# Kernel tuning notes

Measured on AMD Instinct MI355X. Metric: run time of the kernel, lower is better.

## Reference

```python
import jax, jax.numpy as jnp
import numpy as np

N = 4096       # rows (batch * points)
D = 512        # d_model
H = 8          # num_heads


def setup_inputs() -> dict:
    key = jax.random.key(0)
    ks = jax.random.split(key, 11)
    s = 1.0 / np.sqrt(D).astype(np.float32)
    return {
        "x_q": jax.random.normal(ks[0], (N, D), jnp.float32),
        "x_k": jax.random.normal(ks[1], (N, D), jnp.float32),
        "x_v": jax.random.normal(ks[2], (N, D), jnp.float32),
        "Wq": jax.random.normal(ks[3], (D, D), jnp.float32) * s,
        "bq": jax.random.normal(ks[4], (D,), jnp.float32) * s,
        "Wk": jax.random.normal(ks[5], (D, D), jnp.float32) * s,
        "bk": jax.random.normal(ks[6], (D,), jnp.float32) * s,
        "Wv": jax.random.normal(ks[7], (D, D), jnp.float32) * s,
        "bv": jax.random.normal(ks[8], (D,), jnp.float32) * s,
        "Wo": jax.random.normal(ks[9], (D, D), jnp.float32) * s,
        "bo": jax.random.normal(ks[10], (D,), jnp.float32) * s,
    }


def reference(x_q, x_k, x_v, Wq, bq, Wk, bk, Wv, bv, Wo, bo):
    n, d = x_q.shape
    d_k = d // H
    # linear projections
    q = (x_q @ Wq + bq).reshape(n, H, d_k)  # chunk(dim=-1) == head split
    k = (x_k @ Wk + bk).reshape(n, H, d_k)
    v = (x_v @ Wv + bv).reshape(n, H, d_k)
    # channel-wise outer-product attention: scores[n,h,i,j] = q_i * k_j / sqrt(d_k)
    scale = jnp.asarray(1.0 / np.sqrt(d_k), q.dtype)
    scores = q[..., :, None] * k[..., None, :] * scale  # (n, H, d_k, d_k)
    p = jax.nn.softmax(scores, axis=-1)
    # attn output: p @ v over channel axis -> (n, H, d_k)
    x = jnp.einsum('nhij,nhj->nhi', p, v).reshape(n, d)  # head merge (cat dim=-1)
    return (x_q - x) @ Wo + bo
```

## Files before the change

### kernel.cpp

```cpp
#include <hip/hip_runtime.h>
#include <hip/hip_bf16.h>

#define NROWS 4096
#define DMODEL 512
#define NHEAD 8
#define DKH 64
#define ND (NROWS * DMODEL)
#define DD (DMODEL * DMODEL)

typedef unsigned short u16;
typedef __attribute__((ext_vector_type(8))) short short8;
typedef __attribute__((ext_vector_type(4))) float floatx4;

__device__ __forceinline__ u16 f2b(float f) {
    unsigned u = __float_as_uint(f);
    unsigned r = (u + 0x7fffu + ((u >> 16) & 1u)) >> 16;
    return (u16)r;
}
__device__ __forceinline__ float b2f(u16 v) {
    return __uint_as_float(((unsigned)v) << 16);
}
__device__ __forceinline__ void async16(const void* g, void* l) {
    __builtin_amdgcn_global_load_lds(g, l, 16, 0, 0);
}
__device__ __forceinline__ short8 cvt8(float4 a0, float4 a1) {
    short8 av;
    av[0] = f2b(a0.x); av[1] = f2b(a0.y); av[2] = f2b(a0.z); av[3] = f2b(a0.w);
    av[4] = f2b(a1.x); av[5] = f2b(a1.y); av[6] = f2b(a1.z); av[7] = f2b(a1.w);
    return av;
}

__global__ __launch_bounds__(256) void prep(
    const float* __restrict__ W0, const float* __restrict__ W1,
    const float* __restrict__ W2, const float* __restrict__ W3,
    u16* __restrict__ T0, u16* __restrict__ T1, u16* __restrict__ T2,
    u16* __restrict__ T3, const float* __restrict__ x0,
    const float* __restrict__ x1, const float* __restrict__ x2,
    u16* __restrict__ y0, u16* __restrict__ y1, u16* __restrict__ y2) {
    const int bid = blockIdx.x;
    const int tid = threadIdx.x;
    if (bid < 1024) {
        __shared__ float tile[32][33];
        int z = bid >> 8, t = bid & 255;
        const float* W = z == 0 ? W0 : (z == 1 ? W1 : (z == 2 ? W2 : W3));
        u16* T = z == 0 ? T0 : (z == 1 ? T1 : (z == 2 ? T2 : T3));
        int n0 = (t & 15) * 32, k0 = (t >> 4) * 32;
        int tx = tid & 31, ty = tid >> 5;
#pragma unroll
        for (int r = 0; r < 32; r += 8)
            tile[ty + r][tx] = W[(size_t)(k0 + ty + r) * DMODEL + n0 + tx];
        __syncthreads();
#pragma unroll
        for (int r = 0; r < 32; r += 8)
            T[(size_t)(n0 + ty + r) * DMODEL + k0 + tx] = f2b(tile[tx][ty + r]);
    } else {
        int b = bid - 1024;
        int zz = b >> 10;
        const float* s = zz == 0 ? x0 : (zz == 1 ? x1 : x2);
        u16* d = zz == 0 ? y0 : (zz == 1 ? y1 : y2);
        int i = (b & 1023) * 2048 + tid * 8;
        float4 a0 = *(const float4*)(s + i);
        float4 a1 = *(const float4*)(s + i + 4);
        *(short8*)(d + i) = cvt8(a0, a1);
    }
}

__global__ __launch_bounds__(256, 3) void proj3(
    const u16* __restrict__ xqb, const u16* __restrict__ xkb,
    const u16* __restrict__ xvb, const u16* __restrict__ wtq,
    const u16* __restrict__ wtk, const u16* __restrict__ wtv,
    const float* __restrict__ bq, const float* __restrict__ bk,
    const float* __restrict__ bv, u16* __restrict__ Q, u16* __restrict__ K,
    u16* __restrict__ V) {
    __shared__ __align__(16) u16 sA[2][64 * 32];
    __shared__ __align__(16) u16 sB[2][128 * 32];

    const int d = blockIdx.x;
    const int id = (d & 7) * 96 + (d >> 3);
    const int z = id >> 8;
    const int t2 = id & 255;
    const int tileM = (t2 >> 2) * 64;
    const int tileN = (t2 & 3) * 128;

    const u16* A = z == 0 ? xqb : (z == 1 ? xkb : xvb);
    const u16* Bt = z == 0 ? wtq : (z == 1 ? wtk : wtv);
    const float* bias = z == 0 ? bq : (z == 1 ? bk : bv);
    u16* C = z == 0 ? Q : (z == 1 ? K : V);

    const int tid = threadIdx.x;
    const int wave = tid >> 6, lane = tid & 63;
    const int wm = wave >> 1, wn = wave & 1;
    const int lr4 = lane >> 2, ls = lane & 3;
    const int lrow = lane & 15, sk = lane >> 4;

    const int ra = wave * 16 + lr4;
    const int sa = ls ^ ((ra >> 1) & 3);
    const u16* aptr = A + (size_t)(tileM + ra) * 512 + sa * 8;
    const int rb0 = (wave * 2) * 16 + lr4;
    const int rb1 = (wave * 2 + 1) * 16 + lr4;
    const int sb0 = ls ^ ((rb0 >> 1) & 3);
    const int sb1 = ls ^ ((rb1 >> 1) & 3);
    const u16* bptr0 = Bt + (size_t)(tileN + rb0) * 512 + sb0 * 8;
    const u16* bptr1 = Bt + (size_t)(tileN + rb1) * 512 + sb1 * 8;

    floatx4 acc[2][4];
#pragma unroll
    for (int i = 0; i < 2; i++)
#pragma unroll
        for (int j = 0; j < 4; j++) acc[i][j] = (floatx4){0.f, 0.f, 0.f, 0.f};

    async16(aptr, &sA[0][wave * 512]);
    async16(bptr0, &sB[0][wave * 1024]);
    async16(bptr1, &sB[0][wave * 1024 + 512]);
    __syncthreads();

    for (int t = 0; t < 16; ++t) {
        const int cur = t & 1, nxt = cur ^ 1;
        if (t < 15) {
            async16(aptr + (t + 1) * 32, &sA[nxt][wave * 512]);
            async16(bptr0 + (t + 1) * 32, &sB[nxt][wave * 1024]);
            async16(bptr1 + (t + 1) * 32, &sB[nxt][wave * 1024 + 512]);
        }
        short8 afr[2], bfr[4];
#pragma unroll
        for (int mi = 0; mi < 2; ++mi) {
            int r = wm * 32 + mi * 16 + lrow;
            int s = sk ^ ((r >> 1) & 3);
            afr[mi] = *(const short8*)&sA[cur][r * 32 + s * 8];
        }
#pragma unroll
        for (int ni = 0; ni < 4; ++ni) {
            int r = wn * 64 + ni * 16 + lrow;
            int s = sk ^ ((r >> 1) & 3);
            bfr[ni] = *(const short8*)&sB[cur][r * 32 + s * 8];
        }
#pragma unroll
        for (int mi = 0; mi < 2; ++mi)
#pragma unroll
            for (int ni = 0; ni < 4; ++ni)
                acc[mi][ni] = __builtin_amdgcn_mfma_f32_16x16x32_bf16(
                    afr[mi], bfr[ni], acc[mi][ni], 0, 0, 0);
        __syncthreads();
    }

#pragma unroll
    for (int mi = 0; mi < 2; ++mi)
#pragma unroll
        for (int ni = 0; ni < 4; ++ni) {
            int col = tileN + wn * 64 + ni * 16 + lrow;
            float bv_ = bias[col];
#pragma unroll
            for (int r2 = 0; r2 < 4; r2++) {
                int row = tileM + wm * 32 + mi * 16 + sk * 4 + r2;
                C[(size_t)row * 512 + col] = f2b(acc[mi][ni][r2] + bv_);
            }
        }
}

__global__ __launch_bounds__(256) void attn_kernel(
    const u16* __restrict__ Qb, const u16* __restrict__ Kb,
    const u16* __restrict__ Vb, const float* __restrict__ xq,
    u16* __restrict__ Tout) {
    __shared__ float lk[4][64];
    __shared__ float lv[4][64];
    const int wave = threadIdx.x >> 6, lane = threadIdx.x & 63;
    const int p = blockIdx.x * 4 + wave;
    const int n = p >> 3, h = p & 7;
    const size_t base = (size_t)n * DMODEL + h * DKH;

    float qi = b2f(Qb[base + lane]) * 0.125f;
    lk[wave][lane] = b2f(Kb[base + lane]);
    lv[wave][lane] = b2f(Vb[base + lane]);
    __syncthreads();

    float num = 0.f, den = 0.f;
#pragma unroll
    for (int j = 0; j < 64; j += 4) {
        float4 kv = *(const float4*)&lk[wave][j];
        float4 vv = *(const float4*)&lv[wave][j];
        float e0 = __expf(qi * kv.x);
        float e1 = __expf(qi * kv.y);
        float e2 = __expf(qi * kv.z);
        float e3 = __expf(qi * kv.w);
        den += e0 + e1 + e2 + e3;
        num += e0 * vv.x + e1 * vv.y + e2 * vv.z + e3 * vv.w;
    }
    float t = xq[base + lane] - num / den;
    Tout[base + lane] = f2b(t);
}

__global__ __launch_bounds__(256, 2) void out_gemm(const u16* __restrict__ T,
                                                   const u16* __restrict__ wto,
                                                   const float* __restrict__ bo,
                                                   float* __restrict__ C) {
    __shared__ __align__(16) u16 sA[2][2048];
    __shared__ __align__(16) u16 sB[2][2048];
    const int d = blockIdx.x;
    const int id = (d & 7) * 64 + (d >> 3);
    const int tileM = (id >> 3) * 64;
    const int tileN = (id & 7) * 64;

    const int tid = threadIdx.x;
    const int wave = tid >> 6, lane = tid & 63;
    const int wm = wave >> 1, wn = wave & 1;
    const int lr4 = lane >> 2, ls = lane & 3;
    const int lrow = lane & 15, sk = lane >> 4;

    const int r0 = wave * 16 + lr4;
    const int s0 = ls ^ ((r0 >> 1) & 3);
    const u16* aptr = T + (size_t)(tileM + r0) * 512 + s0 * 8;
    const u16* bptr = wto + (size_t)(tileN + r0) * 512 + s0 * 8;

    floatx4 acc[2][2];
#pragma unroll
    for (int i = 0; i < 2; i++)
#pragma unroll
        for (int j = 0; j < 2; j++) acc[i][j] = (floatx4){0.f, 0.f, 0.f, 0.f};

    async16(aptr, &sA[0][wave * 512]);
    async16(bptr, &sB[0][wave * 512]);
    __syncthreads();

    for (int t = 0; t < 16; ++t) {
        const int cur = t & 1, nxt = cur ^ 1;
        if (t < 15) {
            async16(aptr + (t + 1) * 32, &sA[nxt][wave * 512]);
            async16(bptr + (t + 1) * 32, &sB[nxt][wave * 512]);
        }
        short8 afr[2], bfr[2];
#pragma unroll
        for (int mi = 0; mi < 2; ++mi) {
            int r = wm * 32 + mi * 16 + lrow;
            int s = sk ^ ((r >> 1) & 3);
            afr[mi] = *(const short8*)&sA[cur][r * 32 + s * 8];
        }
#pragma unroll
        for (int ni = 0; ni < 2; ++ni) {
            int r = wn * 32 + ni * 16 + lrow;
            int s = sk ^ ((r >> 1) & 3);
            bfr[ni] = *(const short8*)&sB[cur][r * 32 + s * 8];
        }
#pragma unroll
        for (int mi = 0; mi < 2; ++mi)
#pragma unroll
            for (int ni = 0; ni < 2; ++ni)
                acc[mi][ni] = __builtin_amdgcn_mfma_f32_16x16x32_bf16(
                    afr[mi], bfr[ni], acc[mi][ni], 0, 0, 0);
        __syncthreads();
    }

#pragma unroll
    for (int mi = 0; mi < 2; ++mi)
#pragma unroll
        for (int ni = 0; ni < 2; ++ni) {
            int col = tileN + wn * 32 + ni * 16 + lrow;
            float bv = bo[col];
#pragma unroll
            for (int r2 = 0; r2 < 4; r2++) {
                int row = tileM + wm * 32 + mi * 16 + sk * 4 + r2;
                C[(size_t)row * 512 + col] = acc[mi][ni][r2] + bv;
            }
        }
}

extern "C" void kernel_launch(void* const* d_in, const int* in_sizes, int n_in,
                              void* d_out, int out_size, void* d_ws,
                              size_t ws_size, hipStream_t stream) {
    const float* x_q = (const float*)d_in[0];
    const float* x_k = (const float*)d_in[1];
    const float* x_v = (const float*)d_in[2];
    const float* Wq = (const float*)d_in[3];
    const float* bq = (const float*)d_in[4];
    const float* Wk = (const float*)d_in[5];
    const float* bk = (const float*)d_in[6];
    const float* Wv = (const float*)d_in[7];
    const float* bv = (const float*)d_in[8];
    const float* Wo = (const float*)d_in[9];
    const float* bo = (const float*)d_in[10];

    u16* ws = (u16*)d_ws;
    u16* xqb = ws;
    u16* xkb = xqb + ND;
    u16* xvb = xkb + ND;
    u16* wtq = xvb + ND;
    u16* wtk = wtq + DD;
    u16* wtv = wtk + DD;
    u16* wto = wtv + DD;
    u16* Qb = wto + DD;
    u16* Kb = Qb + ND;
    u16* Vb = Kb + ND;
    u16* Tb = Vb + ND;

    prep<<<dim3(4096), 256, 0, stream>>>(Wq, Wk, Wv, Wo, wtq, wtk, wtv, wto,
                                         x_q, x_k, x_v, xqb, xkb, xvb);
    proj3<<<dim3(768), 256, 0, stream>>>(xqb, xkb, xvb, wtq, wtk, wtv, bq, bk,
                                         bv, Qb, Kb, Vb);
    attn_kernel<<<dim3(NROWS * NHEAD / 4), 256, 0, stream>>>(Qb, Kb, Vb, x_q,
                                                             Tb);
    out_gemm<<<dim3(512), 256, 0, stream>>>(Tb, wto, bo, (float*)d_out);
}
```

Before: 138.5 us.

## Fuse fp32-to-bf16 input conversion into projection GEMM and double K tile

The projection GEMM now reads x_q/x_k/x_v as fp32 directly from global memory. It converts them to bf16 in registers and writes them into swizzled LDS, so the separate conversion pass and its bf16 workspace round trip are gone. Both GEMMs move from a K-step of 32 to 64, which halves the number of barriers and loop iterations but doubles LDS use per block. The A operand for the next tile is loaded into registers before the MFMAs and stored after them, which adds register pressure and the cost of reading fp32 directly.

New measurement: 135.3 us, median of 2. 1.02x faster.

```diff
diff --git a/kernel.cpp b/kernel.cpp
--- a/kernel.cpp
+++ b/kernel.cpp
@@ -30,50 +30,35 @@
     return av;
 }
 
-__global__ __launch_bounds__(256) void prep(
+__global__ __launch_bounds__(256) void prep_w(
     const float* __restrict__ W0, const float* __restrict__ W1,
     const float* __restrict__ W2, const float* __restrict__ W3,
     u16* __restrict__ T0, u16* __restrict__ T1, u16* __restrict__ T2,
-    u16* __restrict__ T3, const float* __restrict__ x0,
-    const float* __restrict__ x1, const float* __restrict__ x2,
-    u16* __restrict__ y0, u16* __restrict__ y1, u16* __restrict__ y2) {
-    const int bid = blockIdx.x;
-    const int tid = threadIdx.x;
-    if (bid < 1024) {
-        __shared__ float tile[32][33];
-        int z = bid >> 8, t = bid & 255;
-        const float* W = z == 0 ? W0 : (z == 1 ? W1 : (z == 2 ? W2 : W3));
-        u16* T = z == 0 ? T0 : (z == 1 ? T1 : (z == 2 ? T2 : T3));
-        int n0 = (t & 15) * 32, k0 = (t >> 4) * 32;
-        int tx = tid & 31, ty = tid >> 5;
-#pragma unroll
-        for (int r = 0; r < 32; r += 8)
-            tile[ty + r][tx] = W[(size_t)(k0 + ty + r) * DMODEL + n0 + tx];
-        __syncthreads();
-#pragma unroll
-        for (int r = 0; r < 32; r += 8)
-            T[(size_t)(n0 + ty + r) * DMODEL + k0 + tx] = f2b(tile[tx][ty + r]);
-    } else {
-        int b = bid - 1024;
-        int zz = b >> 10;
-        const float* s = zz == 0 ? x0 : (zz == 1 ? x1 : x2);
-        u16* d = zz == 0 ? y0 : (zz == 1 ? y1 : y2);
-        int i = (b & 1023) * 2048 + tid * 8;
-        float4 a0 = *(const float4*)(s + i);
-        float4 a1 = *(const float4*)(s + i + 4);
-        *(short8*)(d + i) = cvt8(a0, a1);
-    }
+    u16* __restrict__ T3) {
+    __shared__ float tile[32][33];
+    const int z = blockIdx.x >> 8, t = blockIdx.x & 255;
+    const float* W = z == 0 ? W0 : (z == 1 ? W1 : (z == 2 ? W2 : W3));
+    u16* T = z == 0 ? T0 : (z == 1 ? T1 : (z == 2 ? T2 : T3));
+    int n0 = (t & 15) * 32, k0 = (t >> 4) * 32;
+    int tx = threadIdx.x & 31, ty = threadIdx.x >> 5;
+#pragma unroll
+    for (int r = 0; r < 32; r += 8)
+        tile[ty + r][tx] = W[(size_t)(k0 + ty + r) * DMODEL + n0 + tx];
+    __syncthreads();
+#pragma unroll
+    for (int r = 0; r < 32; r += 8)
+        T[(size_t)(n0 + ty + r) * DMODEL + k0 + tx] = f2b(tile[tx][ty + r]);
 }
 
 __global__ __launch_bounds__(256, 3) void proj3(
-    const u16* __restrict__ xqb, const u16* __restrict__ xkb,
-    const u16* __restrict__ xvb, const u16* __restrict__ wtq,
+    const float* __restrict__ xq, const float* __restrict__ xk,
+    const float* __restrict__ xv, const u16* __restrict__ wtq,
     const u16* __restrict__ wtk, const u16* __restrict__ wtv,
     const float* __restrict__ bq, const float* __restrict__ bk,
     const float* __restrict__ bv, u16* __restrict__ Q, u16* __restrict__ K,
     u16* __restrict__ V) {
-    __shared__ __align__(16) u16 sA[2][64 * 32];
-    __shared__ __align__(16) u16 sB[2][128 * 32];
+    __shared__ __align__(16) u16 sA[2][64 * 64];
+    __shared__ __align__(16) u16 sB[2][128 * 64];
 
     const int d = blockIdx.x;
     const int id = (d & 7) * 96 + (d >> 3);
@@ -82,7 +67,7 @@
     const int tileM = (t2 >> 2) * 64;
     const int tileN = (t2 & 3) * 128;
 
-    const u16* A = z == 0 ? xqb : (z == 1 ? xkb : xvb);
+    const float* A = z == 0 ? xq : (z == 1 ? xk : xv);
     const u16* Bt = z == 0 ? wtq : (z == 1 ? wtk : wtv);
     const float* bias = z == 0 ? bq : (z == 1 ? bk : bv);
     u16* C = z == 0 ? Q : (z == 1 ? K : V);
@@ -90,18 +75,26 @@
     const int tid = threadIdx.x;
     const int wave = tid >> 6, lane = tid & 63;
     const int wm = wave >> 1, wn = wave & 1;
-    const int lr4 = lane >> 2, ls = lane & 3;
     const int lrow = lane & 15, sk = lane >> 4;
 
-    const int ra = wave * 16 + lr4;
-    const int sa = ls ^ ((ra >> 1) & 3);
-    const u16* aptr = A + (size_t)(tileM + ra) * 512 + sa * 8;
-    const int rb0 = (wave * 2) * 16 + lr4;
-    const int rb1 = (wave * 2 + 1) * 16 + lr4;
-    const int sb0 = ls ^ ((rb0 >> 1) & 3);
-    const int sb1 = ls ^ ((rb1 >> 1) & 3);
-    const u16* bptr0 = Bt + (size_t)(tileN + rb0) * 512 + sb0 * 8;
-    const u16* bptr1 = Bt + (size_t)(tileN + rb1) * 512 + sb1 * 8;
+    const int arow = tid >> 2, apair = tid & 3;
+    const int axor = (arow >> 1) & 7;
+    const int as0 = (2 * apair) ^ axor;
+    const int as1 = (2 * apair + 1) ^ axor;
+    const float* aptr = A + (size_t)(tileM + arow) * 512 + apair * 16;
+    const int aw0 = arow * 64 + as0 * 8;
+    const int aw1 = arow * 64 + as1 * 8;
+
+    const u16* bptr[4];
+    int bdst[4];
+#pragma unroll
+    for (int i = 0; i < 4; i++) {
+        int c = wave * 4 + i;
+        int row = c * 8 + (lane >> 3);
+        int s = (lane & 7) ^ ((row >> 1) & 7);
+        bptr[i] = Bt + (size_t)(tileN + row) * 512 + s * 8;
+        bdst[i] = c * 512;
+    }
 
     floatx4 acc[2][4];
 #pragma unroll
@@ -109,37 +102,59 @@
 #pragma unroll
         for (int j = 0; j < 4; j++) acc[i][j] = (floatx4){0.f, 0.f, 0.f, 0.f};
 
-    async16(aptr, &sA[0][wave * 512]);
-    async16(bptr0, &sB[0][wave * 1024]);
-    async16(bptr1, &sB[0][wave * 1024 + 512]);
+#pragma unroll
+    for (int i = 0; i < 4; i++) async16(bptr[i], &sB[0][bdst[i]]);
+    {
+        float4 a0 = *(const float4*)aptr;
+        float4 a1 = *(const float4*)(aptr + 4);
+        float4 a2 = *(const float4*)(aptr + 8);
+        float4 a3 = *(const float4*)(aptr + 12);
+        *(short8*)&sA[0][aw0] = cvt8(a0, a1);
+        *(short8*)&sA[0][aw1] = cvt8(a2, a3);
+    }
     __syncthreads();
 
-    for (int t = 0; t < 16; ++t) {
+    for (int t = 0; t < 8; ++t) {
         const int cur = t & 1, nxt = cur ^ 1;
-        if (t < 15) {
-            async16(aptr + (t + 1) * 32, &sA[nxt][wave * 512]);
-            async16(bptr0 + (t + 1) * 32, &sB[nxt][wave * 1024]);
-            async16(bptr1 + (t + 1) * 32, &sB[nxt][wave * 1024 + 512]);
-        }
-        short8 afr[2], bfr[4];
-#pragma unroll
-        for (int mi = 0; mi < 2; ++mi) {
-            int r = wm * 32 + mi * 16 + lrow;
-            int s = sk ^ ((r >> 1) & 3);
-            afr[mi] = *(const short8*)&sA[cur][r * 32 + s * 8];
-        }
-#pragma unroll
-        for (int ni = 0; ni < 4; ++ni) {
-            int r = wn * 64 + ni * 16 + lrow;
-            int s = sk ^ ((r >> 1) & 3);
-            bfr[ni] = *(const short8*)&sB[cur][r * 32 + s * 8];
-        }
-#pragma unroll
-        for (int mi = 0; mi < 2; ++mi)
-#pragma unroll
-            for (int ni = 0; ni < 4; ++ni)
-                acc[mi][ni] = __builtin_amdgcn_mfma_f32_16x16x32_bf16(
-                    afr[mi], bfr[ni], acc[mi][ni], 0, 0, 0);
+        float4 n0, n1, n2, n3;
+        if (t < 7) {
+            const float* p = aptr + (t + 1) * 64;
+            n0 = *(const float4*)p;
+            n1 = *(const float4*)(p + 4);
+            n2 = *(const float4*)(p + 8);
+            n3 = *(const float4*)(p + 12);
+#pragma unroll
+            for (int i = 0; i < 4; i++)
+                async16(bptr[i] + (t + 1) * 64, &sB[nxt][bdst[i]]);
+        }
+        short8 afr[2][2], bfr[2][4];
+#pragma unroll
+        for (int kk = 0; kk < 2; ++kk) {
+#pragma unroll
+            for (int mi = 0; mi < 2; ++mi) {
+                int r = wm * 32 + mi * 16 + lrow;
+                int s = (kk * 4 + sk) ^ ((r >> 1) & 7);
+                afr[kk][mi] = *(const short8*)&sA[cur][r * 64 + s * 8];
+            }
+#pragma unroll
+            for (int ni = 0; ni < 4; ++ni) {
+                int r = wn * 64 + ni * 16 + lrow;
+                int s = (kk * 4 + sk) ^ ((r >> 1) & 7);
+                bfr[kk][ni] = *(const short8*)&sB[cur][r * 64 + s * 8];
+            }
+        }
+#pragma unroll
+        for (int kk = 0; kk < 2; ++kk)
+#pragma unroll
+            for (int mi = 0; mi < 2; ++mi)
+#pragma unroll
+                for (int ni = 0; ni < 4; ++ni)
+                    acc[mi][ni] = __builtin_amdgcn_mfma_f32_16x16x32_bf16(
+                        afr[kk][mi], bfr[kk][ni], acc[mi][ni], 0, 0, 0);
+        if (t < 7) {
+            *(short8*)&sA[nxt][aw0] = cvt8(n0, n1);
+            *(short8*)&sA[nxt][aw1] = cvt8(n2, n3);
+        }
         __syncthreads();
     }
 
@@ -193,8 +208,8 @@
                                                    const u16* __restrict__ wto,
                                                    const float* __restrict__ bo,
                                                    float* __restrict__ C) {
-    __shared__ __align__(16) u16 sA[2][2048];
-    __shared__ __align__(16) u16 sB[2][2048];
+    __shared__ __align__(16) u16 sA[2][64 * 64];
+    __shared__ __align__(16) u16 sB[2][64 * 64];
     const int d = blockIdx.x;
     const int id = (d & 7) * 64 + (d >> 3);
     const int tileM = (id >> 3) * 64;
@@ -203,13 +218,20 @@
     const int tid = threadIdx.x;
     const int wave = tid >> 6, lane = tid & 63;
     const int wm = wave >> 1, wn = wave & 1;
-    const int lr4 = lane >> 2, ls = lane & 3;
     const int lrow = lane & 15, sk = lane >> 4;
 
-    const int r0 = wave * 16 + lr4;
-    const int s0 = ls ^ ((r0 >> 1) & 3);
-    const u16* aptr = T + (size_t)(tileM + r0) * 512 + s0 * 8;
-    const u16* bptr = wto + (size_t)(tileN + r0) * 512 + s0 * 8;
+    const u16* aptr[2];
+    const u16* bptr[2];
+    int dst[2];
+#pragma unroll
+    for (int i = 0; i < 2; i++) {
+        int c = wave * 2 + i;
+        int row = c * 8 + (lane >> 3);
+        int s = (lane & 7) ^ ((row >> 1) & 7);
+        aptr[i] = T + (size_t)(tileM + row) * 512 + s * 8;
+        bptr[i] = wto + (size_t)(tileN + row) * 512 + s * 8;
+        dst[i] = c * 512;
+    }
 
     floatx4 acc[2][2];
 #pragma unroll
@@ -217,35 +239,46 @@
 #pragma unroll
         for (int j = 0; j < 2; j++) acc[i][j] = (floatx4){0.f, 0.f, 0.f, 0.f};
 
-    async16(aptr, &sA[0][wave * 512]);
-    async16(bptr, &sB[0][wave * 512]);
+#pragma unroll
+    for (int i = 0; i < 2; i++) {
+        async16(aptr[i], &sA[0][dst[i]]);
+        async16(bptr[i], &sB[0][dst[i]]);
+    }
     __syncthreads();
 
-    for (int t = 0; t < 16; ++t) {
+    for (int t = 0; t < 8; ++t) {
         const int cur = t & 1, nxt = cur ^ 1;
-        if (t < 15) {
-            async16(aptr + (t + 1) * 32, &sA[nxt][wave * 512]);
-            async16(bptr + (t + 1) * 32, &sB[nxt][wave * 512]);
-        }
-        short8 afr[2], bfr[2];
-#pragma unroll
-        for (int mi = 0; mi < 2; ++mi) {
-            int r = wm * 32 + mi * 16 + lrow;
-            int s = sk ^ ((r >> 1) & 3);
-            afr[mi] = *(const short8*)&sA[cur][r * 32 + s * 8];
-        }
-#pragma unroll
-        for (int ni = 0; ni < 2; ++ni) {
-            int r = wn * 32 + ni * 16 + lrow;
-            int s = sk ^ ((r >> 1) & 3);
-            bfr[ni] = *(const short8*)&sB[cur][r * 32 + s * 8];
-        }
-#pragma unroll
-        for (int mi = 0; mi < 2; ++mi)
-#pragma unroll
-            for (int ni = 0; ni < 2; ++ni)
-                acc[mi][ni] = __builtin_amdgcn_mfma_f32_16x16x32_bf16(
-                    afr[mi], bfr[ni], acc[mi][ni], 0, 0, 0);
+        if (t < 7) {
+#pragma unroll
+            for (int i = 0; i < 2; i++) {
+                async16(aptr[i] + (t + 1) * 64, &sA[nxt][dst[i]]);
+                async16(bptr[i] + (t + 1) * 64, &sB[nxt][dst[i]]);
+            }
+        }
+        short8 afr[2][2], bfr[2][2];
+#pragma unroll
+        for (int kk = 0; kk < 2; ++kk) {
+#pragma unroll
+            for (int mi = 0; mi < 2; ++mi) {
+                int r = wm * 32 + mi * 16 + lrow;
+                int s = (kk * 4 + sk) ^ ((r >> 1) & 7);
+                afr[kk][mi] = *(const short8*)&sA[cur][r * 64 + s * 8];
+            }
+#pragma unroll
+            for (int ni = 0; ni < 2; ++ni) {
+                int r = wn * 32 + ni * 16 + lrow;
+                int s = (kk * 4 + sk) ^ ((r >> 1) & 7);
+                bfr[kk][ni] = *(const short8*)&sB[cur][r * 64 + s * 8];
+            }
+        }
+#pragma unroll
+        for (int kk = 0; kk < 2; ++kk)
+#pragma unroll
+            for (int mi = 0; mi < 2; ++mi)
+#pragma unroll
+                for (int ni = 0; ni < 2; ++ni)
+                    acc[mi][ni] = __builtin_amdgcn_mfma_f32_16x16x32_bf16(
+                        afr[kk][mi], bfr[kk][ni], acc[mi][ni], 0, 0, 0);
         __syncthreads();
     }
 
@@ -279,10 +312,7 @@
     const float* bo = (const float*)d_in[10];
 
     u16* ws = (u16*)d_ws;
-    u16* xqb = ws;
-    u16* xkb = xqb + ND;
-    u16* xvb = xkb + ND;
-    u16* wtq = xvb + ND;
+    u16* wtq = ws;
     u16* wtk = wtq + DD;
     u16* wtv = wtk + DD;
     u16* wto = wtv + DD;
@@ -291,9 +321,8 @@
     u16* Vb = Kb + ND;
     u16* Tb = Vb + ND;
 
-    prep<<<dim3(4096), 256, 0, stream>>>(Wq, Wk, Wv, Wo, wtq, wtk, wtv, wto,
-                                         x_q, x_k, x_v, xqb, xkb, xvb);
-    proj3<<<dim3(768), 256, 0, stream>>>(xqb, xkb, xvb, wtq, wtk, wtv, bq, bk,
+    prep_w<<<dim3(1024), 256, 0, stream>>>(Wq, Wk, Wv, Wo, wtq, wtk, wtv, wto);
+    proj3<<<dim3(768), 256, 0, stream>>>(x_q, x_k, x_v, wtq, wtk, wtv, bq, bk,
                                          bv, Qb, Kb, Vb);
     attn_kernel<<<dim3(NROWS * NHEAD / 4), 256, 0, stream>>>(Qb, Kb, Vb, x_q,
                                                              Tb);
```
